# Kernel tuning notes

Measured on AMD Instinct MI355X. Metric: run time of the kernel, lower is better.

## Reference

```python
import jax, jax.numpy as jnp
import numpy as np

NODES, NFEAT = 128, 256


def setup_inputs() -> dict:
    key = jax.random.key(0)
    k1, k2, k3, k4, k5, k6 = jax.random.split(key, 6)
    B = 512
    x = jax.random.normal(k1, (B, NODES, NFEAT), dtype=jnp.float32)
    adj = jax.random.uniform(k2, (B, NODES, NODES), dtype=jnp.float32)
    # GraphConvolution(nfeat, nfeat): weight [nfeat, nfeat], bias [nfeat]
    s = 1.0 / np.sqrt(NFEAT)
    gcn_w = jax.random.uniform(k3, (NFEAT, NFEAT), minval=-s, maxval=s, dtype=jnp.float32)
    gcn_b = jax.random.uniform(k4, (NFEAT,), minval=-s, maxval=s, dtype=jnp.float32)
    # fc: Linear(nfeat*nodes, nfeat), torch layout [out, in]
    s2 = 1.0 / np.sqrt(NFEAT * NODES)
    fc_w = jax.random.uniform(k5, (NFEAT, NFEAT * NODES), minval=-s2, maxval=s2, dtype=jnp.float32)
    fc_b = jax.random.uniform(k6, (NFEAT,), minval=-s2, maxval=s2, dtype=jnp.float32)
    return {"x": x, "adj": adj, "gcn_w": gcn_w, "gcn_b": gcn_b, "fc_w": fc_w, "fc_b": fc_b}


def reference(x, adj, gcn_w, gcn_b, fc_w, fc_b):
    B = x.shape[0]
    # Per-sample loop GCN fused as batched matmuls:
    # support = X @ W ; out = A @ support + b
    support = jnp.einsum('bnf,fg->bng', x, gcn_w)          # [B, nodes, nfeat]
    mid = jnp.einsum('bnm,bmg->bng', adj, support) + gcn_b  # [B, nodes, nfeat]
    # cat along dim0 then reshape(-1, nfeat*nodes) == per-graph flatten
    flat = mid.reshape(B, NODES * NFEAT)
    output = flat @ fc_w.T + fc_b                           # [B, nfeat]
    useful_input = x[:, 0, :]                               # [B, nfeat]
    return (output, useful_input, output)
```

## Files before the change

kernel.cpp:

```cpp
#include <hip/hip_runtime.h>

#define NODES 128
#define NFEAT 256
#define BATCH 512
#define KTOT  (NODES * NFEAT)
#define SPLIT 64
#define KCH   (KTOT / SPLIT)

typedef __bf16 bf16_t;
typedef bf16_t bf16x8 __attribute__((ext_vector_type(8)));
typedef float  f32x4  __attribute__((ext_vector_type(4)));

#define BK    32
#define LDK   40
#define BK2   64
#define LDK2  72
#define LDM   136
#define TILE  128

__device__ __forceinline__ void bar() {
    asm volatile("s_waitcnt lgkmcnt(0)\n\ts_barrier" ::: "memory");
}

__device__ __forceinline__ bf16x8 cvt8(const float4 a, const float4 b) {
    bf16x8 t;
    t[0] = (bf16_t)a.x; t[1] = (bf16_t)a.y; t[2] = (bf16_t)a.z; t[3] = (bf16_t)a.w;
    t[4] = (bf16_t)b.x; t[5] = (bf16_t)b.y; t[6] = (bf16_t)b.z; t[7] = (bf16_t)b.w;
    return t;
}

struct XT { float4 v[4]; };
__device__ __forceinline__ void xload(const float* __restrict__ src, int ld, int k0,
                                      int tid, XT& t) {
#pragma unroll
    for (int i = 0; i < 2; i++) {
        int f = tid + i * 256, r = f >> 2, c = f & 3;
        t.v[2 * i]     = *(const float4*)(src + (size_t)r * ld + k0 + c * 8);
        t.v[2 * i + 1] = *(const float4*)(src + (size_t)r * ld + k0 + c * 8 + 4);
    }
}
__device__ __forceinline__ void xstore(bf16_t* __restrict__ dst, int tid, const XT& t) {
#pragma unroll
    for (int i = 0; i < 2; i++) {
        int f = tid + i * 256, r = f >> 2, c = f & 3;
        *(bf16x8*)(dst + r * LDK + c * 8) = cvt8(t.v[2 * i], t.v[2 * i + 1]);
    }
}

struct XT2 { float4 v[8]; };
__device__ __forceinline__ void xload2(const float* __restrict__ src, int ld, int k0,
                                       int tid, XT2& t) {
#pragma unroll
    for (int i = 0; i < 4; i++) {
        int f = tid + i * 256, r = f >> 3, c = f & 7;
        t.v[2 * i]     = *(const float4*)(src + (size_t)r * ld + k0 + c * 8);
        t.v[2 * i + 1] = *(const float4*)(src + (size_t)r * ld + k0 + c * 8 + 4);
    }
}
__device__ __forceinline__ void xstore2(bf16_t* __restrict__ dst, int tid, const XT2& t) {
#pragma unroll
    for (int i = 0; i < 4; i++) {
        int f = tid + i * 256, r = f >> 3, c = f & 7;
        *(bf16x8*)(dst + r * LDK2 + c * 8) = cvt8(t.v[2 * i], t.v[2 * i + 1]);
    }
}

struct AT2 { bf16x8 v[4]; };
__device__ __forceinline__ void aload2(const bf16_t* __restrict__ src, int ld, int k0,
                                       int tid, AT2& t) {
#pragma unroll
    for (int i = 0; i < 4; i++) {
        int f = tid + i * 256, r = f >> 3, c = f & 7;
        t.v[i] = *(const bf16x8*)(src + (size_t)r * ld + k0 + c * 8);
    }
}
__device__ __forceinline__ void astore2(bf16_t* __restrict__ dst, int tid, const AT2& t) {
#pragma unroll
    for (int i = 0; i < 4; i++) {
        int f = tid + i * 256, r = f >> 3, c = f & 7;
        *(bf16x8*)(dst + r * LDK2 + c * 8) = t.v[i];
    }
}

__global__ __launch_bounds__(256)
void k_wt(const float* __restrict__ w, bf16_t* __restrict__ wT) {
    const int g0 = blockIdx.x * 4;
    const int k  = threadIdx.x;
    const float4 v = *(const float4*)(w + (size_t)k * NFEAT + g0);
    wT[(size_t)(g0 + 0) * NFEAT + k] = (bf16_t)v.x;
    wT[(size_t)(g0 + 1) * NFEAT + k] = (bf16_t)v.y;
    wT[(size_t)(g0 + 2) * NFEAT + k] = (bf16_t)v.z;
    wT[(size_t)(g0 + 3) * NFEAT + k] = (bf16_t)v.w;
}

__global__ __launch_bounds__(256, 3)
void k_fused12(const float* __restrict__ x, const float* __restrict__ adj,
               const bf16_t* __restrict__ wT, const float* __restrict__ gcn_b,
               bf16_t* __restrict__ mid) {
    __shared__ __align__(16) bf16_t As[TILE * LDK];
    __shared__ __align__(16) bf16_t Sb[TILE * LDM];
    const int n0  = blockIdx.x * TILE;
    const int b   = blockIdx.y;
    const int tid = threadIdx.x;
    const int lane = tid & 63, w = tid >> 6, wm = w & 1, wn = w >> 1;
    const int l15 = lane & 15, q = lane >> 4;
    const float* xb   = x   + (size_t)b * NODES * NFEAT;
    const float* adjb = adj + (size_t)b * NODES * NODES;

    const bf16_t* wrow[4];
#pragma unroll
    for (int j = 0; j < 4; j++)
        wrow[j] = wT + (size_t)(n0 + wn * 64 + j * 16 + l15) * NFEAT + q * 8;

    f32x4 acc[4][4] = {};
    {
        XT r0, rn, r2;
        xload(xb, NFEAT, 0, tid, r0);
        xload(xb, NFEAT, BK, tid, rn);
        bf16x8 bcur[4], bnxt[4];
#pragma unroll
        for (int j = 0; j < 4; j++) bcur[j] = *(const bf16x8*)(wrow[j]);
        xstore(As, tid, r0);
        bar();
        for (int k0 = 0; k0 < NFEAT; k0 += BK) {
            const bool in1 = (k0 + BK)   < NFEAT;
            const bool in2 = (k0 + 2*BK) < NFEAT;
            if (in2) xload(xb, NFEAT, k0 + 2*BK, tid, r2);
            const int knc = in1 ? k0 + BK : 0;
#pragma unroll
            for (int j = 0; j < 4; j++) bnxt[j] = *(const bf16x8*)(wrow[j] + knc);
            bf16x8 a[4];
#pragma unroll
            for (int i = 0; i < 4; i++)
                a[i] = *(const bf16x8*)(As + (wm * 64 + i * 16 + l15) * LDK + q * 8);
#pragma unroll
            for (int i = 0; i < 4; i++)
#pragma unroll
                for (int j = 0; j < 4; j++)
                    acc[i][j] = __builtin_amdgcn_mfma_f32_16x16x32_bf16(a[i], bcur[j], acc[i][j], 0, 0, 0);
            bar();
            if (in1) xstore(As, tid, rn);
            rn = r2;
#pragma unroll
            for (int j = 0; j < 4; j++) bcur[j] = bnxt[j];
            bar();
        }
    }

    XT a0, a1, a2;
    xload(adjb, NODES, 0, tid, a0);
    xload(adjb, NODES, BK, tid, a1);
#pragma unroll
    for (int i = 0; i < 4; i++)
#pragma unroll
        for (int j = 0; j < 4; j++)
#pragma unroll
            for (int r = 0; r < 4; r++) {
                int m = wm * 64 + i * 16 + q * 4 + r;
                int g = wn * 64 + j * 16 + l15;
                Sb[g * LDM + m] = (bf16_t)acc[i][j][r];
            }
    bar();
    xstore(As, tid, a0);
    bar();

    f32x4 acc2[4][4] = {};
    for (int k0 = 0; k0 < NODES; k0 += BK) {
        const bool in1 = (k0 + BK)   < NODES;
        const bool in2 = (k0 + 2*BK) < NODES;
        if (in2) xload(adjb, NODES, k0 + 2*BK, tid, a2);
        bf16x8 a[4], bb[4];
#pragma unroll
        for (int i = 0; i < 4; i++)
            a[i] = *(const bf16x8*)(As + (wm * 64 + i * 16 + l15) * LDK + q * 8);
#pragma unroll
        for (int j = 0; j < 4; j++)
            bb[j] = *(const bf16x8*)(Sb + (wn * 64 + j * 16 + l15) * LDM + k0 + q * 8);
#pragma unroll
        for (int i = 0; i < 4; i++)
#pragma unroll
            for (int j = 0; j < 4; j++)
                acc2[i][j] = __builtin_amdgcn_mfma_f32_16x16x32_bf16(a[i], bb[j], acc2[i][j], 0, 0, 0);
        bar();
        if (in1) xstore(As, tid, a1);
        a1 = a2;
        bar();
    }
    bf16_t* outb = mid + (size_t)b * NODES * NFEAT;
#pragma unroll
    for (int j = 0; j < 4; j++) {
        int g = n0 + wn * 64 + j * 16 + l15;
        float bias = gcn_b[g];
#pragma unroll
        for (int i = 0; i < 4; i++)
#pragma unroll
            for (int r = 0; r < 4; r++) {
                int node = wm * 64 + i * 16 + q * 4 + r;
                outb[(size_t)node * NFEAT + g] = (bf16_t)(acc2[i][j][r] + bias);
            }
    }
}

__global__ __launch_bounds__(256, 3)
void k_out(const bf16_t* __restrict__ flat, const float* __restrict__ fcw,
           bf16_t* __restrict__ part) {
    __shared__ __align__(16) bf16_t As[TILE * LDK2];
    __shared__ __align__(16) bf16_t Bs[TILE * LDK2];
    const int m0 = blockIdx.x * TILE;
    const int n0 = blockIdx.y * TILE;
    const int kb = blockIdx.z * KCH, kend = kb + KCH;
    const int tid = threadIdx.x;
    const int lane = tid & 63, w = tid >> 6, wm = w & 1, wn = w >> 1;
    const int l15 = lane & 15, q = lane >> 4;
    f32x4 acc[4][4] = {};
    const bf16_t* fa = flat + (size_t)m0 * KTOT;
    const float*  fb = fcw + (size_t)n0 * KTOT;

    AT2 at; aload2(fa, KTOT, kb, tid, at);
    XT2 bt; xload2(fb, KTOT, kb, tid, bt);
    astore2(As, tid, at);
    xstore2(Bs, tid, bt);
    bar();
    for (int k0 = kb; k0 < kend; k0 += BK2) {
        const int kn = k0 + BK2;
        const bool in = kn < kend;
        AT2 an; XT2 bn;
        if (in) { aload2(fa, KTOT, kn, tid, an); xload2(fb, KTOT, kn, tid, bn); }
#pragma unroll
        for (int kk = 0; kk < BK2; kk += BK) {
            bf16x8 a[4], bbf[4];
#pragma unroll
            for (int i = 0; i < 4; i++)
                a[i] = *(const bf16x8*)(As + (wm * 64 + i * 16 + l15) * LDK2 + kk + q * 8);
#pragma unroll
            for (int j = 0; j < 4; j++)
                bbf[j] = *(const bf16x8*)(Bs + (wn * 64 + j * 16 + l15) * LDK2 + kk + q * 8);
#pragma unroll
            for (int i = 0; i < 4; i++)
#pragma unroll
                for (int j = 0; j < 4; j++)
                    acc[i][j] = __builtin_amdgcn_mfma_f32_16x16x32_bf16(a[i], bbf[j], acc[i][j], 0, 0, 0);
        }
        bar();
        if (in) { astore2(As, tid, an); xstore2(Bs, tid, bn); }
        bar();
    }
    bf16_t* pb = part + (size_t)blockIdx.z * BATCH * NFEAT;
#pragma unroll
    for (int i = 0; i < 4; i++)
#pragma unroll
        for (int j = 0; j < 4; j++)
#pragma unroll
            for (int r = 0; r < 4; r++) {
                int bt_ = m0 + wm * 64 + i * 16 + q * 4 + r;
                int o   = n0 + wn * 64 + j * 16 + l15;
                pb[(size_t)bt_ * NFEAT + o] = (bf16_t)acc[i][j][r];
            }
}

__global__ __launch_bounds__(256)
void k_reduce(const bf16_t* __restrict__ part, const float* __restrict__ fc_b,
              const float* __restrict__ x, float* __restrict__ out) {
    const int g8 = (blockIdx.x * 256 + threadIdx.x) * 8;
    const int o = g8 & (NFEAT - 1), b = g8 >> 8;
    float s[8];
    const float4 c0 = *(const float4*)(fc_b + o);
    const float4 c1 = *(const float4*)(fc_b + o + 4);
    s[0] = c0.x; s[1] = c0.y; s[2] = c0.z; s[3] = c0.w;
    s[4] = c1.x; s[5] = c1.y; s[6] = c1.z; s[7] = c1.w;
#pragma unroll 8
    for (int i = 0; i < SPLIT; i++) {
        bf16x8 p = *(const bf16x8*)(part + (size_t)i * BATCH * NFEAT + g8);
#pragma unroll
        for (int j = 0; j < 8; j++) s[j] += (float)p[j];
    }
    float4 o0 = make_float4(s[0], s[1], s[2], s[3]);
    float4 o1 = make_float4(s[4], s[5], s[6], s[7]);
    *(float4*)(out + g8)     = o0;
    *(float4*)(out + g8 + 4) = o1;
    *(float4*)(out + 2 * BATCH * NFEAT + g8)     = o0;
    *(float4*)(out + 2 * BATCH * NFEAT + g8 + 4) = o1;
    const float4 x0 = *(const float4*)(x + (size_t)b * NODES * NFEAT + o);
    const float4 x1 = *(const float4*)(x + (size_t)b * NODES * NFEAT + o + 4);
    *(float4*)(out + BATCH * NFEAT + g8)     = x0;
    *(float4*)(out + BATCH * NFEAT + g8 + 4) = x1;
}

extern "C" void kernel_launch(void* const* d_in, const int* in_sizes, int n_in,
                              void* d_out, int out_size, void* d_ws, size_t ws_size,
                              hipStream_t stream) {
    const float* x     = (const float*)d_in[0];
    const float* adj   = (const float*)d_in[1];
    const float* gcn_w = (const float*)d_in[2];
    const float* gcn_b = (const float*)d_in[3];
    const float* fc_w  = (const float*)d_in[4];
    const float* fc_b  = (const float*)d_in[5];
    float* out = (float*)d_out;

    bf16_t* wT   = (bf16_t*)d_ws;
    bf16_t* mid  = (bf16_t*)((char*)d_ws + 131072);
    bf16_t* part = (bf16_t*)((char*)d_ws + 131072 + (size_t)BATCH * NODES * NFEAT * 2);

    k_wt     <<<dim3(64), dim3(256), 0, stream>>>(gcn_w, wT);
    k_fused12<<<dim3(2, BATCH), dim3(256), 0, stream>>>(x, adj, wT, gcn_b, mid);
    k_out    <<<dim3(4, 2, SPLIT), dim3(256), 0, stream>>>(mid, fc_w, part);
    k_reduce <<<dim3(64), dim3(256), 0, stream>>>(part, fc_b, x, out);
}
```

Before: 203.7 us.

## Double-buffer LDS in k_out, batch two graphs per fused block, rescalarize reduce

k_out now keeps two LDS buffers and prefetches two k-steps ahead, which removes one barrier per iteration at the cost of doubled shared memory and occupancy lowered to 2. k_fused12 processes two batch samples per block with half the grid, so the W^T fragment pointers are reused across both. k_reduce switches from 8-wide vector loads to 2 scalar elements per thread over four times as many blocks, which likely makes its memory accesses less efficient. The bf16x4 typedef is added but never used.

Measured after the change: 222.3 us. +9.1%, slower.

```diff
diff --git a/kernel.cpp b/kernel.cpp
--- a/kernel.cpp
+++ b/kernel.cpp
@@ -8,6 +8,7 @@
 #define KCH   (KTOT / SPLIT)
 
 typedef __bf16 bf16_t;
+typedef bf16_t bf16x4 __attribute__((ext_vector_type(4)));
 typedef bf16_t bf16x8 __attribute__((ext_vector_type(8)));
 typedef float  f32x4  __attribute__((ext_vector_type(4)));
 
@@ -100,115 +101,119 @@
     __shared__ __align__(16) bf16_t As[TILE * LDK];
     __shared__ __align__(16) bf16_t Sb[TILE * LDM];
     const int n0  = blockIdx.x * TILE;
-    const int b   = blockIdx.y;
     const int tid = threadIdx.x;
     const int lane = tid & 63, w = tid >> 6, wm = w & 1, wn = w >> 1;
     const int l15 = lane & 15, q = lane >> 4;
-    const float* xb   = x   + (size_t)b * NODES * NFEAT;
-    const float* adjb = adj + (size_t)b * NODES * NODES;
 
     const bf16_t* wrow[4];
 #pragma unroll
     for (int j = 0; j < 4; j++)
         wrow[j] = wT + (size_t)(n0 + wn * 64 + j * 16 + l15) * NFEAT + q * 8;
 
-    f32x4 acc[4][4] = {};
-    {
-        XT r0, rn, r2;
-        xload(xb, NFEAT, 0, tid, r0);
-        xload(xb, NFEAT, BK, tid, rn);
-        bf16x8 bcur[4], bnxt[4];
-#pragma unroll
-        for (int j = 0; j < 4; j++) bcur[j] = *(const bf16x8*)(wrow[j]);
-        xstore(As, tid, r0);
+    for (int bb = 0; bb < 2; bb++) {
+        const int b = blockIdx.y * 2 + bb;
+        const float* xb   = x   + (size_t)b * NODES * NFEAT;
+        const float* adjb = adj + (size_t)b * NODES * NODES;
+
+        f32x4 acc[4][4] = {};
+        {
+            XT r0, rn, r2;
+            xload(xb, NFEAT, 0, tid, r0);
+            xload(xb, NFEAT, BK, tid, rn);
+            bf16x8 bcur[4], bnxt[4];
+#pragma unroll
+            for (int j = 0; j < 4; j++) bcur[j] = *(const bf16x8*)(wrow[j]);
+            bar();
+            xstore(As, tid, r0);
+            bar();
+            for (int k0 = 0; k0 < NFEAT; k0 += BK) {
+                const bool in1 = (k0 + BK)   < NFEAT;
+                const bool in2 = (k0 + 2*BK) < NFEAT;
+                if (in2) xload(xb, NFEAT, k0 + 2*BK, tid, r2);
+                const int knc = in1 ? k0 + BK : 0;
+#pragma unroll
+                for (int j = 0; j < 4; j++) bnxt[j] = *(const bf16x8*)(wrow[j] + knc);
+                bf16x8 a[4];
+#pragma unroll
+                for (int i = 0; i < 4; i++)
+                    a[i] = *(const bf16x8*)(As + (wm * 64 + i * 16 + l15) * LDK + q * 8);
+#pragma unroll
+                for (int i = 0; i < 4; i++)
+#pragma unroll
+                    for (int j = 0; j < 4; j++)
+                        acc[i][j] = __builtin_amdgcn_mfma_f32_16x16x32_bf16(a[i], bcur[j], acc[i][j], 0, 0, 0);
+                bar();
+                if (in1) xstore(As, tid, rn);
+                rn = r2;
+#pragma unroll
+                for (int j = 0; j < 4; j++) bcur[j] = bnxt[j];
+                bar();
+            }
+        }
+
+        XT a0, a1, a2;
+        xload(adjb, NODES, 0, tid, a0);
+        xload(adjb, NODES, BK, tid, a1);
+#pragma unroll
+        for (int i = 0; i < 4; i++)
+#pragma unroll
+            for (int j = 0; j < 4; j++)
+#pragma unroll
+                for (int rr = 0; rr < 4; rr++) {
+                    int m = wm * 64 + i * 16 + q * 4 + rr;
+                    int g = wn * 64 + j * 16 + l15;
+                    Sb[g * LDM + m] = (bf16_t)acc[i][j][rr];
+                }
         bar();
-        for (int k0 = 0; k0 < NFEAT; k0 += BK) {
-            const bool in1 = (k0 + BK)   < NFEAT;
-            const bool in2 = (k0 + 2*BK) < NFEAT;
-            if (in2) xload(xb, NFEAT, k0 + 2*BK, tid, r2);
-            const int knc = in1 ? k0 + BK : 0;
-#pragma unroll
-            for (int j = 0; j < 4; j++) bnxt[j] = *(const bf16x8*)(wrow[j] + knc);
-            bf16x8 a[4];
+        xstore(As, tid, a0);
+        bar();
+
+        f32x4 acc2[4][4] = {};
+        for (int k0 = 0; k0 < NODES; k0 += BK) {
+            const bool in1 = (k0 + BK)   < NODES;
+            const bool in2 = (k0 + 2*BK) < NODES;
+            if (in2) xload(adjb, NODES, k0 + 2*BK, tid, a2);
+            bf16x8 a[4], bb2[4];
 #pragma unroll
             for (int i = 0; i < 4; i++)
                 a[i] = *(const bf16x8*)(As + (wm * 64 + i * 16 + l15) * LDK + q * 8);
 #pragma unroll
+            for (int j = 0; j < 4; j++)
+                bb2[j] = *(const bf16x8*)(Sb + (wn * 64 + j * 16 + l15) * LDM + k0 + q * 8);
+#pragma unroll
             for (int i = 0; i < 4; i++)
 #pragma unroll
                 for (int j = 0; j < 4; j++)
-                    acc[i][j] = __builtin_amdgcn_mfma_f32_16x16x32_bf16(a[i], bcur[j], acc[i][j], 0, 0, 0);
+                    acc2[i][j] = __builtin_amdgcn_mfma_f32_16x16x32_bf16(a[i], bb2[j], acc2[i][j], 0, 0, 0);
             bar();
-            if (in1) xstore(As, tid, rn);
-            rn = r2;
-#pragma unroll
-            for (int j = 0; j < 4; j++) bcur[j] = bnxt[j];
+            if (in1) xstore(As, tid, a1);
+            a1 = a2;
             bar();
         }
-    }
-
-    XT a0, a1, a2;
-    xload(adjb, NODES, 0, tid, a0);
-    xload(adjb, NODES, BK, tid, a1);
-#pragma unroll
-    for (int i = 0; i < 4; i++)
-#pragma unroll
-        for (int j = 0; j < 4; j++)
-#pragma unroll
-            for (int r = 0; r < 4; r++) {
-                int m = wm * 64 + i * 16 + q * 4 + r;
-                int g = wn * 64 + j * 16 + l15;
-                Sb[g * LDM + m] = (bf16_t)acc[i][j][r];
-            }
-    bar();
-    xstore(As, tid, a0);
-    bar();
-
-    f32x4 acc2[4][4] = {};
-    for (int k0 = 0; k0 < NODES; k0 += BK) {
-        const bool in1 = (k0 + BK)   < NODES;
-        const bool in2 = (k0 + 2*BK) < NODES;
-        if (in2) xload(adjb, NODES, k0 + 2*BK, tid, a2);
-        bf16x8 a[4], bb[4];
-#pragma unroll
-        for (int i = 0; i < 4; i++)
-            a[i] = *(const bf16x8*)(As + (wm * 64 + i * 16 + l15) * LDK + q * 8);
-#pragma unroll
-        for (int j = 0; j < 4; j++)
-            bb[j] = *(const bf16x8*)(Sb + (wn * 64 + j * 16 + l15) * LDM + k0 + q * 8);
-#pragma unroll
-        for (int i = 0; i < 4; i++)
-#pragma unroll
-            for (int j = 0; j < 4; j++)
-                acc2[i][j] = __builtin_amdgcn_mfma_f32_16x16x32_bf16(a[i], bb[j], acc2[i][j], 0, 0, 0);
-        bar();
-        if (in1) xstore(As, tid, a1);
-        a1 = a2;
-        bar();
-    }
-    bf16_t* outb = mid + (size_t)b * NODES * NFEAT;
-#pragma unroll
-    for (int j = 0; j < 4; j++) {
-        int g = n0 + wn * 64 + j * 16 + l15;
-        float bias = gcn_b[g];
-#pragma unroll
-        for (int i = 0; i < 4; i++)
-#pragma unroll
-            for (int r = 0; r < 4; r++) {
-                int node = wm * 64 + i * 16 + q * 4 + r;
-                outb[(size_t)node * NFEAT + g] = (bf16_t)(acc2[i][j][r] + bias);
-            }
-    }
-}
-
-__global__ __launch_bounds__(256, 3)
+        bf16_t* outb = mid + (size_t)b * NODES * NFEAT;
+#pragma unroll
+        for (int j = 0; j < 4; j++) {
+            int g = n0 + wn * 64 + j * 16 + l15;
+            float bias = gcn_b[g];
+#pragma unroll
+            for (int i = 0; i < 4; i++)
+#pragma unroll
+                for (int rr = 0; rr < 4; rr++) {
+                    int node = wm * 64 + i * 16 + q * 4 + rr;
+                    outb[(size_t)node * NFEAT + g] = (bf16_t)(acc2[i][j][rr] + bias);
+                }
+        }
+    }
+}
+
+__global__ __launch_bounds__(256, 2)
 void k_out(const bf16_t* __restrict__ flat, const float* __restrict__ fcw,
            bf16_t* __restrict__ part) {
-    __shared__ __align__(16) bf16_t As[TILE * LDK2];
-    __shared__ __align__(16) bf16_t Bs[TILE * LDK2];
+    __shared__ __align__(16) bf16_t As[2][TILE * LDK2];
+    __shared__ __align__(16) bf16_t Bs[2][TILE * LDK2];
     const int m0 = blockIdx.x * TILE;
     const int n0 = blockIdx.y * TILE;
-    const int kb = blockIdx.z * KCH, kend = kb + KCH;
+    const int kb = blockIdx.z * KCH;
     const int tid = threadIdx.x;
     const int lane = tid & 63, w = tid >> 6, wm = w & 1, wn = w >> 1;
     const int l15 = lane & 15, q = lane >> 4;
@@ -216,33 +221,40 @@
     const bf16_t* fa = flat + (size_t)m0 * KTOT;
     const float*  fb = fcw + (size_t)n0 * KTOT;
 
-    AT2 at; aload2(fa, KTOT, kb, tid, at);
-    XT2 bt; xload2(fb, KTOT, kb, tid, bt);
-    astore2(As, tid, at);
-    xstore2(Bs, tid, bt);
+    AT2 acur, anxt; XT2 bcur, bnxt;
+    aload2(fa, KTOT, kb, tid, acur);
+    xload2(fb, KTOT, kb, tid, bcur);
+    aload2(fa, KTOT, kb + BK2, tid, anxt);
+    xload2(fb, KTOT, kb + BK2, tid, bnxt);
+    astore2(As[0], tid, acur);
+    xstore2(Bs[0], tid, bcur);
     bar();
-    for (int k0 = kb; k0 < kend; k0 += BK2) {
-        const int kn = k0 + BK2;
-        const bool in = kn < kend;
-        AT2 an; XT2 bn;
-        if (in) { aload2(fa, KTOT, kn, tid, an); xload2(fb, KTOT, kn, tid, bn); }
+#pragma unroll 2
+    for (int k = 0; k < 8; k++) {
+        const bool in2 = k + 2 < 8;
+        AT2 a2; XT2 b2;
+        if (in2) { aload2(fa, KTOT, kb + (k + 2) * BK2, tid, a2);
+                   xload2(fb, KTOT, kb + (k + 2) * BK2, tid, b2); }
 #pragma unroll
         for (int kk = 0; kk < BK2; kk += BK) {
             bf16x8 a[4], bbf[4];
 #pragma unroll
             for (int i = 0; i < 4; i++)
-                a[i] = *(const bf16x8*)(As + (wm * 64 + i * 16 + l15) * LDK2 + kk + q * 8);
+                a[i] = *(const bf16x8*)(&As[k & 1][(wm * 64 + i * 16 + l15) * LDK2 + kk + q * 8]);
 #pragma unroll
             for (int j = 0; j < 4; j++)
-                bbf[j] = *(const bf16x8*)(Bs + (wn * 64 + j * 16 + l15) * LDK2 + kk + q * 8);
+                bbf[j] = *(const bf16x8*)(&Bs[k & 1][(wn * 64 + j * 16 + l15) * LDK2 + kk + q * 8]);
 #pragma unroll
             for (int i = 0; i < 4; i++)
 #pragma unroll
                 for (int j = 0; j < 4; j++)
                     acc[i][j] = __builtin_amdgcn_mfma_f32_16x16x32_bf16(a[i], bbf[j], acc[i][j], 0, 0, 0);
         }
-        bar();
-        if (in) { astore2(As, tid, an); xstore2(Bs, tid, bn); }
+        if (k + 1 < 8) {
+            astore2(As[(k + 1) & 1], tid, anxt);
+            xstore2(Bs[(k + 1) & 1], tid, bnxt);
+        }
+        anxt = a2; bnxt = b2;
         bar();
     }
     bf16_t* pb = part + (size_t)blockIdx.z * BATCH * NFEAT;
@@ -261,29 +273,19 @@
 __global__ __launch_bounds__(256)
 void k_reduce(const bf16_t* __restrict__ part, const float* __restrict__ fc_b,
               const float* __restrict__ x, float* __restrict__ out) {
-    const int g8 = (blockIdx.x * 256 + threadIdx.x) * 8;
-    const int o = g8 & (NFEAT - 1), b = g8 >> 8;
-    float s[8];
-    const float4 c0 = *(const float4*)(fc_b + o);
-    const float4 c1 = *(const float4*)(fc_b + o + 4);
-    s[0] = c0.x; s[1] = c0.y; s[2] = c0.z; s[3] = c0.w;
-    s[4] = c1.x; s[5] = c1.y; s[6] = c1.z; s[7] = c1.w;
-#pragma unroll 8
+    const int g2 = (blockIdx.x * 256 + threadIdx.x) * 2;
+    const int o = g2 & (NFEAT - 1), b = g2 >> 8;
+    float s0 = fc_b[o], s1 = fc_b[o + 1];
+#pragma unroll 16
     for (int i = 0; i < SPLIT; i++) {
-        bf16x8 p = *(const bf16x8*)(part + (size_t)i * BATCH * NFEAT + g8);
-#pragma unroll
-        for (int j = 0; j < 8; j++) s[j] += (float)p[j];
-    }
-    float4 o0 = make_float4(s[0], s[1], s[2], s[3]);
-    float4 o1 = make_float4(s[4], s[5], s[6], s[7]);
-    *(float4*)(out + g8)     = o0;
-    *(float4*)(out + g8 + 4) = o1;
-    *(float4*)(out + 2 * BATCH * NFEAT + g8)     = o0;
-    *(float4*)(out + 2 * BATCH * NFEAT + g8 + 4) = o1;
-    const float4 x0 = *(const float4*)(x + (size_t)b * NODES * NFEAT + o);
-    const float4 x1 = *(const float4*)(x + (size_t)b * NODES * NFEAT + o + 4);
-    *(float4*)(out + BATCH * NFEAT + g8)     = x0;
-    *(float4*)(out + BATCH * NFEAT + g8 + 4) = x1;
+        bf16_t p0 = part[(size_t)i * BATCH * NFEAT + g2];
+        bf16_t p1 = part[(size_t)i * BATCH * NFEAT + g2 + 1];
+        s0 += (float)p0; s1 += (float)p1;
+    }
+    out[g2] = s0; out[g2 + 1] = s1;
+    out[2 * BATCH * NFEAT + g2] = s0; out[2 * BATCH * NFEAT + g2 + 1] = s1;
+    out[BATCH * NFEAT + g2]     = x[(size_t)b * NODES * NFEAT + o];
+    out[BATCH * NFEAT + g2 + 1] = x[(size_t)b * NODES * NFEAT + o + 1];
 }
 
 extern "C" void kernel_launch(void* const* d_in, const int* in_sizes, int n_in,
@@ -302,7 +304,7 @@
     bf16_t* part = (bf16_t*)((char*)d_ws + 131072 + (size_t)BATCH * NODES * NFEAT * 2);
 
     k_wt     <<<dim3(64), dim3(256), 0, stream>>>(gcn_w, wT);
-    k_fused12<<<dim3(2, BATCH), dim3(256), 0, stream>>>(x, adj, wT, gcn_b, mid);
+    k_fused12<<<dim3(2, 256), dim3(256), 0, stream>>>(x, adj, wT, gcn_b, mid);
     k_out    <<<dim3(4, 2, SPLIT), dim3(256), 0, stream>>>(mid, fc_w, part);
-    k_reduce <<<dim3(64), dim3(256), 0, stream>>>(part, fc_b, x, out);
-}
+    k_reduce <<<dim3(256), dim3(256), 0, stream>>>(part, fc_b, x, out);
+}
```
